# Performance work log

Measured on AMD Instinct MI355X. Metric: run time of the kernel, lower is better.

## Reference

```python
import jax, jax.numpy as jnp
import numpy as np

B, T, K, H = 2, 2048, 1024, 16


def setup_inputs() -> dict:
    key = jax.random.key(0)
    ks = jax.random.split(key, 9)
    sc = 0.02
    return {
        "x": jax.random.normal(ks[0], (B, T, K), dtype=jnp.float32),
        "Wq_w": jax.random.normal(ks[1], (K, K), dtype=jnp.float32) * sc,
        "Wq_b": jax.random.normal(ks[2], (K,), dtype=jnp.float32) * sc,
        "Wk_w": jax.random.normal(ks[3], (K, K), dtype=jnp.float32) * sc,
        "Wk_b": jax.random.normal(ks[4], (K,), dtype=jnp.float32) * sc,
        "Wv_w": jax.random.normal(ks[5], (K, K), dtype=jnp.float32) * sc,
        "Wv_b": jax.random.normal(ks[6], (K,), dtype=jnp.float32) * sc,
        "Wo_w": jax.random.normal(ks[7], (K, K), dtype=jnp.float32) * sc,
        "Wo_b": jax.random.normal(ks[8], (K,), dtype=jnp.float32) * sc,
    }


def reference(x, Wq_w, Wq_b, Wk_w, Wk_b, Wv_w, Wv_b, Wo_w, Wo_b):
    b, t, k = x.shape
    h = H
    s = k // h
    # nn.Linear: y = x @ W^T + b
    q = x @ Wq_w.T + Wq_b
    kk = x @ Wk_w.T + Wk_b
    v = x @ Wv_w.T + Wv_b
    # [b, t, h, s] -> [b, h, t, s]
    q = q.reshape(b, t, h, s).transpose(0, 2, 1, 3)
    kk = kk.reshape(b, t, h, s).transpose(0, 2, 1, 3)
    v = v.reshape(b, t, h, s).transpose(0, 2, 1, 3)
    # scores [b, h, t, t]
    dot = jnp.einsum("bhqd,bhkd->bhqk", q, kk)
    # causal mask: upper triangle (offset=1) set to -inf BEFORE scaling
    causal = jnp.tril(jnp.ones((t, t), dtype=bool))
    dot = jnp.where(causal, dot, -jnp.inf)
    # NOTE: original scales by sqrt(k) (full model dim), not sqrt(head_dim)
    dot = dot / jnp.sqrt(jnp.asarray(k, dot.dtype))
    attn = jax.nn.softmax(dot, axis=-1)
    out = jnp.einsum("bhqk,bhkd->bhqd", attn, v)  # [b, h, t, s]
    out = out.transpose(0, 2, 1, 3).reshape(b, t, k)
    return out @ Wo_w.T + Wo_b
```

## Files before the change

### kernel.cpp

```cpp
#include <hip/hip_runtime.h>

typedef unsigned short u16;
typedef unsigned int u32;
typedef __bf16 bf16x8 __attribute__((ext_vector_type(8)));
typedef float f32x4 __attribute__((ext_vector_type(4)));
typedef unsigned short u16x8 __attribute__((ext_vector_type(8)));
typedef unsigned int u32x4 __attribute__((ext_vector_type(4)));

#define B_ 2
#define T_ 2048
#define K_ 1024
#define H_ 16
#define S_ 64
#define MKC 4194304
#define QSCALE 0.04508422f

__device__ __forceinline__ u16 f2bf(float f) {
  unsigned int u = __builtin_bit_cast(unsigned int, f);
  u += 0x7fffu + ((u >> 16) & 1u);
  return (u16)(u >> 16);
}

__device__ __forceinline__ f32x4 MFMA(bf16x8 a, bf16x8 b, f32x4 c) {
  return __builtin_amdgcn_mfma_f32_16x16x32_bf16(a, b, c, 0, 0, 0);
}

__device__ __forceinline__ void gld16(const void* g, void* l) {
  __builtin_amdgcn_global_load_lds((const __attribute__((address_space(1))) void*)g,
                                   (__attribute__((address_space(3))) void*)l, 16, 0, 0);
}

template <int N>
__device__ __forceinline__ void waitv() {
  asm volatile("s_waitcnt vmcnt(%0)" ::"i"(N) : "memory");
}
__device__ __forceinline__ void memfence_barrier() {
  asm volatile("" ::: "memory");
  __builtin_amdgcn_s_barrier();
}
__device__ __forceinline__ float fmax3(float a, float b, float c) {
  return fmaxf(fmaxf(a, b), c);
}

__global__ __launch_bounds__(256) void cvt_all(const float* __restrict__ x,
                                               const float* __restrict__ W0,
                                               const float* __restrict__ W1,
                                               const float* __restrict__ W2,
                                               const float* __restrict__ W3,
                                               u16* __restrict__ xb,
                                               u16* __restrict__ wb) {
  const int i = blockIdx.x * 256 + threadIdx.x;
  const float* src;
  u16* dst;
  if (i < 524288) {
    src = x + (size_t)i * 8;
    dst = xb + (size_t)i * 8;
  } else {
    const int j = i - 524288;
    const int sel = j >> 17;
    const float* W = sel == 0 ? W0 : sel == 1 ? W1 : sel == 2 ? W2 : W3;
    src = W + (size_t)(j & 131071) * 8;
    dst = wb + (size_t)j * 8;
  }
  const float4* s = (const float4*)src;
  float4 f0 = s[0], f1 = s[1];
  u16x8 p;
  p[0] = f2bf(f0.x); p[1] = f2bf(f0.y); p[2] = f2bf(f0.z); p[3] = f2bf(f0.w);
  p[4] = f2bf(f1.x); p[5] = f2bf(f1.y); p[6] = f2bf(f1.z); p[7] = f2bf(f1.w);
  *(u16x8*)dst = p;
}

template <int OMODE, int BN>
__global__ __launch_bounds__(256) void gemm16(const u16* __restrict__ A,
                                              const u16* __restrict__ Bm,
                                              const float* __restrict__ b0,
                                              const float* __restrict__ b1,
                                              const float* __restrict__ b2,
                                              void* __restrict__ C0,
                                              int M, int N, int K) {
  constexpr int NF = BN / 32;
  constexpr int SOPS = 2 + BN / 64;
  __shared__ u16 As[2][128 * 32];
  __shared__ u16 Bs[2][BN * 32];
  const int bm = blockIdx.x * 128;
  const int bn = blockIdx.y * BN;
  const int tid = threadIdx.x;
  const int w = tid >> 6, lane = tid & 63;
  const int wr = (w >> 1) * 64, wc = (w & 1) * (BN / 2);
  const int lr = lane & 15, g = lane >> 4;
  const int lk = g * 8;
  const int srow = lane >> 2, scol = (lane & 3) * 8;

  f32x4 acc[4][NF] = {};

  auto stg = [&](int buf, int k0) {
#pragma unroll
    for (int i = 0; i < 2; ++i) {
      const int rbase = (i * 4 + w) * 16;
      gld16(A + (size_t)(bm + rbase + srow) * K + k0 + scol, &As[buf][rbase * 32]);
    }
#pragma unroll
    for (int i = 0; i < BN / 64; ++i) {
      const int rbase = (i * 4 + w) * 16;
      gld16(Bm + (size_t)(bn + rbase + srow) * K + k0 + scol, &Bs[buf][rbase * 32]);
    }
  };

  stg(0, 0);
  const int NK = K >> 5;
  for (int kk = 0; kk < NK; ++kk) {
    const int buf = kk & 1;
    const bool pf = (kk + 1 < NK);
    if (pf) {
      stg(buf ^ 1, (kk + 1) * 32);
      waitv<SOPS>();
    } else {
      waitv<0>();
    }
    __builtin_amdgcn_s_barrier();
    bf16x8 af[4], bfr[NF];
#pragma unroll
    for (int m = 0; m < 4; ++m)
      af[m] = *(const bf16x8*)&As[buf][(wr + m * 16 + lr) * 32 + lk];
#pragma unroll
    for (int n = 0; n < NF; ++n)
      bfr[n] = *(const bf16x8*)&Bs[buf][(wc + n * 16 + lr) * 32 + lk];
#pragma unroll
    for (int m = 0; m < 4; ++m)
#pragma unroll
      for (int n = 0; n < NF; ++n)
        acc[m][n] = MFMA(af[m], bfr[n], acc[m][n]);
    memfence_barrier();
  }

  const int sel = (OMODE == 2) ? 0 : (bn >> 10);
  const float* bp = (OMODE == 2) ? b0 : (sel == 0 ? b0 : sel == 1 ? b1 : b2);
#pragma unroll
  for (int n = 0; n < NF; ++n) {
    const int col = bn + wc + n * 16 + lr;
    const float bv = bp[(OMODE == 2) ? col : (col & 1023)];
#pragma unroll
    for (int m = 0; m < 4; ++m) {
#pragma unroll
      for (int r = 0; r < 4; ++r) {
        const int row = bm + wr + m * 16 + g * 4 + r;
        float v = acc[m][n][r] + bv;
        if (OMODE == 2) {
          ((float*)C0)[(size_t)row * N + col] = v;
        } else {
          u16* dst = (u16*)C0;
          const int cc = col & 1023;
          if (sel == 2) {
            const int bb = row >> 11, t = row & 2047, hh = cc >> 6, ss = cc & 63;
            dst[(size_t)2 * MKC + (((size_t)(bb * H_ + hh) * S_ + ss) << 11) + t] = f2bf(v);
          } else {
            if (sel == 0) v *= QSCALE;
            dst[(size_t)sel * MKC + (size_t)row * 1024 + cc] = f2bf(v);
          }
        }
      }
    }
  }
}

__global__ __launch_bounds__(256) void attn_fwd(const u16* __restrict__ Q,
                                                const u16* __restrict__ Kb,
                                                const u16* __restrict__ Vt,
                                                u16* __restrict__ O) {
  __shared__ u16 Ks[2][64 * 64];
  __shared__ u16 Vs[2][64 * 64];
  const int tid = threadIdx.x;
  const int w = tid >> 6, lane = tid & 63;
  const int qh = lane & 15;
  const int g = lane >> 4;
  const int bh = blockIdx.x;
  const int b = bh >> 4, h = bh & 15;
  const int yy = blockIdx.y;

  const int srow = lane >> 3;
  const int sl8 = ((lane & 7) ^ srow) * 8;
  int kvp[2];
#pragma unroll
  for (int i = 0; i < 2; ++i) {
    const int rho = w * 16 + i * 8 + srow;
    const int a = rho >> 4;
    kvp[i] = ((a >> 1) << 5) | (((rho >> 2) & 3) << 3) | ((a & 1) << 2) | (rho & 3);
  }
  const int ksw = qh & 7;
  u16x8 ov;
#pragma unroll
  for (int i = 0; i < 8; ++i) ov[i] = 0x3F80;
  const bf16x8 ones = __builtin_bit_cast(bf16x8, ov);

  for (int seg = 0; seg < 2; ++seg) {
    const int qtile = seg ? (31 - yy) : yy;
    const int qb = qtile * 64;
    const int qw = qb + w * 16;
    const int myq = qw + qh;
    const int nk = qtile + 1;

    const size_t qoff = (size_t)(b * T_ + qw + qh) * K_ + h * S_ + g * 8;
    const bf16x8 bq0 = *(const bf16x8*)(Q + qoff);
    const bf16x8 bq1 = *(const bf16x8*)(Q + qoff + 32);

    const u16* kq0 = Kb + (size_t)(b * T_ + kvp[0]) * K_ + h * S_ + sl8;
    const u16* kq1 = Kb + (size_t)(b * T_ + kvp[1]) * K_ + h * S_ + sl8;
    const u16* vq0 = Vt + (size_t)(bh * S_ + w * 16 + srow) * T_ + sl8;
    const u16* vq1 = Vt + (size_t)(bh * S_ + w * 16 + 8 + srow) * T_ + sl8;

    auto stageK = [&](int buf) {
      gld16(kq0, &Ks[buf][(w * 16) * 64]);
      gld16(kq1, &Ks[buf][(w * 16 + 8) * 64]);
      kq0 += 64 * K_; kq1 += 64 * K_;
    };
    auto stageV = [&](int buf) {
      gld16(vq0, &Vs[buf][(w * 16) * 64]);
      gld16(vq1, &Vs[buf][(w * 16 + 8) * 64]);
      vq0 += 64; vq1 += 64;
    };

    float m = -INFINITY;
    f32x4 o[4] = {};
    f32x4 o_l = {};
    f32x4 sA[4], sB[4];

    auto QKT = [&](int buf, f32x4 (&sO)[4]) {
      __builtin_amdgcn_s_setprio(1);
#pragma unroll
      for (int a = 0; a < 4; ++a) {
        const u16* kr = &Ks[buf][(a * 16 + qh) * 64];
        const bf16x8 kf0 = *(const bf16x8*)(kr + ((g ^ ksw) * 8));
        const bf16x8 kf1 = *(const bf16x8*)(kr + (((4 + g) ^ ksw) * 8));
        f32x4 z = {0.f, 0.f, 0.f, 0.f};
        z = MFMA(kf0, bq0, z);
        sO[a] = MFMA(kf1, bq1, z);
      }
      __builtin_amdgcn_s_setprio(0);
    };

    auto SMPV = [&](f32x4 (&sIn)[4], int buf, int k0) {
      float p[4][4];
      if (k0 + 63 > qw) {
        const int thr = myq - k0 - (g << 3);
#pragma unroll
        for (int a = 0; a < 4; ++a)
#pragma unroll
          for (int r = 0; r < 4; ++r) {
            const int C = ((a >> 1) << 5) + ((a & 1) << 2) + r;
            p[a][r] = (C <= thr) ? sIn[a][r] : -INFINITY;
          }
      } else {
#pragma unroll
        for (int a = 0; a < 4; ++a)
#pragma unroll
          for (int r = 0; r < 4; ++r) p[a][r] = sIn[a][r];
      }
      float x0 = fmax3(p[0][0], p[0][1], p[0][2]);
      float x1 = fmax3(p[0][3], p[1][0], p[1][1]);
      float x2 = fmax3(p[1][2], p[1][3], p[2][0]);
      float x3 = fmax3(p[2][1], p[2][2], p[2][3]);
      float x4 = fmax3(p[3][0], p[3][1], p[3][2]);
      float vmax = fmax3(fmax3(x0, x1, x2), x3, fmaxf(x4, p[3][3]));
      vmax = fmaxf(vmax, __shfl_xor(vmax, 16));
      vmax = fmaxf(vmax, __shfl_xor(vmax, 32));

      if (__any(vmax > m + 11.5f)) {
        const float mnew = fmaxf(m, vmax);
        const float alpha = __builtin_amdgcn_exp2f(m - mnew);
        m = mnew;
        float aR[4];
#pragma unroll
        for (int r = 0; r < 4; ++r) aR[r] = __shfl(alpha, 4 * g + r);
#pragma unroll
        for (int nn = 0; nn < 4; ++nn)
#pragma unroll
          for (int r = 0; r < 4; ++r) o[nn][r] *= aR[r];
#pragma unroll
        for (int r = 0; r < 4; ++r) o_l[r] *= aR[r];
      }

#pragma unroll
      for (int a = 0; a < 4; ++a)
#pragma unroll
        for (int r = 0; r < 4; ++r)
          p[a][r] = __builtin_amdgcn_exp2f(p[a][r] - m);

      __builtin_amdgcn_s_setprio(1);
#pragma unroll
      for (int c = 0; c < 2; ++c) {
        u32 t0, t1, t2, t3;
        asm("v_cvt_pk_bf16_f32 %0, %1, %2" : "=v"(t0) : "v"(p[2 * c][0]), "v"(p[2 * c][1]));
        asm("v_cvt_pk_bf16_f32 %0, %1, %2" : "=v"(t1) : "v"(p[2 * c][2]), "v"(p[2 * c][3]));
        asm("v_cvt_pk_bf16_f32 %0, %1, %2" : "=v"(t2) : "v"(p[2 * c + 1][0]), "v"(p[2 * c + 1][1]));
        asm("v_cvt_pk_bf16_f32 %0, %1, %2" : "=v"(t3) : "v"(p[2 * c + 1][2]), "v"(p[2 * c + 1][3]));
        u32x4 tv; tv[0] = t0; tv[1] = t1; tv[2] = t2; tv[3] = t3;
        const bf16x8 pa = __builtin_bit_cast(bf16x8, tv);
        o_l = MFMA(pa, ones, o_l);
#pragma unroll
        for (int nn = 0; nn < 4; ++nn) {
          const bf16x8 vf =
              *(const bf16x8*)(&Vs[buf][(16 * nn + qh) * 64] + (((c * 4 + g) ^ ksw) * 8));
          o[nn] = MFMA(pa, vf, o[nn]);
        }
      }
      __builtin_amdgcn_s_setprio(0);
    };

    stageK(0); stageV(0);
    waitv<0>();
    __builtin_amdgcn_s_barrier();
    QKT(0, sA);
    if (nk > 1) { stageK(1); stageV(1); }

    int kt = 0;
    for (;;) {
      {
        const bool hn = kt + 1 < nk;
        if (hn) waitv<2>(); else waitv<0>();
        __builtin_amdgcn_s_barrier();
        if (hn) { QKT(1, sB); if (kt + 2 < nk) stageK(0); }
        SMPV(sA, 0, kt * 64);
        memfence_barrier();
        if (kt + 2 < nk) stageV(0);
        if (!hn) break;
        ++kt;
      }
      {
        const bool hn = kt + 1 < nk;
        if (hn) waitv<2>(); else waitv<0>();
        __builtin_amdgcn_s_barrier();
        if (hn) { QKT(0, sA); if (kt + 2 < nk) stageK(1); }
        SMPV(sB, 1, kt * 64);
        memfence_barrier();
        if (kt + 2 < nk) stageV(1);
        if (!hn) break;
        ++kt;
      }
    }

#pragma unroll
    for (int r = 0; r < 4; ++r) {
      const float inv = 1.f / o_l[r];
      const size_t row = (size_t)(b * T_ + qw + 4 * g + r);
#pragma unroll
      for (int nn = 0; nn < 4; ++nn)
        O[row * K_ + h * S_ + nn * 16 + qh] = f2bf(o[nn][r] * inv);
    }
  }
}

extern "C" void kernel_launch(void* const* d_in, const int* in_sizes, int n_in,
                              void* d_out, int out_size, void* d_ws, size_t ws_size,
                              hipStream_t stream) {
  (void)in_sizes; (void)n_in; (void)out_size; (void)ws_size;
  const float* x  = (const float*)d_in[0];
  const float* Wq = (const float*)d_in[1];
  const float* bq = (const float*)d_in[2];
  const float* Wk = (const float*)d_in[3];
  const float* bk = (const float*)d_in[4];
  const float* Wv = (const float*)d_in[5];
  const float* bv = (const float*)d_in[6];
  const float* Wo = (const float*)d_in[7];
  const float* bo = (const float*)d_in[8];
  float* out = (float*)d_out;

  const size_t MK = (size_t)MKC;
  const size_t WK = (size_t)K_ * K_;
  u16* Qb  = (u16*)d_ws;
  u16* Kbf = Qb + MK;
  u16* Vtb = Kbf + MK;
  u16* AO  = Vtb + MK;
  u16* xb  = AO + MK;
  u16* Wqkv = xb + MK;
  u16* Wob  = Wqkv + 3 * WK;

  dim3 blk(256);
  cvt_all<<<dim3(4096), blk, 0, stream>>>(x, Wq, Wk, Wv, Wo, xb, Wqkv);
  gemm16<3, 128><<<dim3(32, 24), blk, 0, stream>>>(xb, Wqkv, bq, bk, bv, Qb,
                                                   B_ * T_, 3 * K_, K_);
  attn_fwd<<<dim3(B_ * H_, 16), blk, 0, stream>>>(Qb, Kbf, Vtb, AO);
  gemm16<2, 64><<<dim3(32, 16), blk, 0, stream>>>(AO, Wob, bo, bo, bo, out,
                                                  B_ * T_, K_, K_);
}
```

Baseline: 105.7 us.

## Split long causal query tiles across two blocks and merge partials

Attention work is rebalanced. Before, each block paired query tile y with tile 31-y. Now the 16 longest query tiles have their KV range split into two halves handled by separate blocks, and the 16 shorter tiles run as single blocks, giving 48 blocks per head instead of 16. Split blocks write normalized bf16 partial outputs plus row max and sum into the reused xb workspace, and a new merge kernel combines them with log-sum-exp weights. The aim is more parallelism and shorter per-block critical paths, at the cost of an extra launch, extra global traffic, and bf16 rounding of the partials.

Result: slower. 110.3 us (+4.4%).

```diff
diff --git a/kernel.cpp b/kernel.cpp
--- a/kernel.cpp
+++ b/kernel.cpp
@@ -14,11 +14,16 @@
 #define S_ 64
 #define MKC 4194304
 #define QSCALE 0.04508422f
+#define PSTRIDE 4352
 
 __device__ __forceinline__ u16 f2bf(float f) {
   unsigned int u = __builtin_bit_cast(unsigned int, f);
   u += 0x7fffu + ((u >> 16) & 1u);
   return (u16)(u >> 16);
+}
+__device__ __forceinline__ float bf2f(u16 u) {
+  u32 x = ((u32)u) << 16;
+  return __builtin_bit_cast(float, x);
 }
 
 __device__ __forceinline__ f32x4 MFMA(bf16x8 a, bf16x8 b, f32x4 c) {
@@ -166,7 +171,8 @@
 __global__ __launch_bounds__(256) void attn_fwd(const u16* __restrict__ Q,
                                                 const u16* __restrict__ Kb,
                                                 const u16* __restrict__ Vt,
-                                                u16* __restrict__ O) {
+                                                u16* __restrict__ O,
+                                                u16* __restrict__ part) {
   __shared__ u16 Ks[2][64 * 64];
   __shared__ u16 Vs[2][64 * 64];
   const int tid = threadIdx.x;
@@ -175,7 +181,25 @@
   const int g = lane >> 4;
   const int bh = blockIdx.x;
   const int b = bh >> 4, h = bh & 15;
-  const int yy = blockIdx.y;
+  const int j = blockIdx.y;
+  int y, k_lo, k_hi;
+  if (j < 32) {
+    y = 31 - (j >> 1);
+    const int h0 = (y + 2) >> 1;
+    k_lo = (j & 1) ? h0 : 0;
+    k_hi = (j & 1) ? (y + 1) : h0;
+  } else {
+    y = 47 - j;
+    k_lo = 0;
+    k_hi = y + 1;
+  }
+  const int qb = y * 64;
+  const int qw = qb + w * 16;
+  const int myq = qw + qh;
+
+  const size_t qoff = (size_t)(b * T_ + qw + qh) * K_ + h * S_ + g * 8;
+  const bf16x8 bq0 = *(const bf16x8*)(Q + qoff);
+  const bf16x8 bq1 = *(const bf16x8*)(Q + qoff + 32);
 
   const int srow = lane >> 3;
   const int sl8 = ((lane & 7) ^ srow) * 8;
@@ -192,152 +216,142 @@
   for (int i = 0; i < 8; ++i) ov[i] = 0x3F80;
   const bf16x8 ones = __builtin_bit_cast(bf16x8, ov);
 
-  for (int seg = 0; seg < 2; ++seg) {
-    const int qtile = seg ? (31 - yy) : yy;
-    const int qb = qtile * 64;
-    const int qw = qb + w * 16;
-    const int myq = qw + qh;
-    const int nk = qtile + 1;
-
-    const size_t qoff = (size_t)(b * T_ + qw + qh) * K_ + h * S_ + g * 8;
-    const bf16x8 bq0 = *(const bf16x8*)(Q + qoff);
-    const bf16x8 bq1 = *(const bf16x8*)(Q + qoff + 32);
-
-    const u16* kq0 = Kb + (size_t)(b * T_ + kvp[0]) * K_ + h * S_ + sl8;
-    const u16* kq1 = Kb + (size_t)(b * T_ + kvp[1]) * K_ + h * S_ + sl8;
-    const u16* vq0 = Vt + (size_t)(bh * S_ + w * 16 + srow) * T_ + sl8;
-    const u16* vq1 = Vt + (size_t)(bh * S_ + w * 16 + 8 + srow) * T_ + sl8;
-
-    auto stageK = [&](int buf) {
-      gld16(kq0, &Ks[buf][(w * 16) * 64]);
-      gld16(kq1, &Ks[buf][(w * 16 + 8) * 64]);
-      kq0 += 64 * K_; kq1 += 64 * K_;
-    };
-    auto stageV = [&](int buf) {
-      gld16(vq0, &Vs[buf][(w * 16) * 64]);
-      gld16(vq1, &Vs[buf][(w * 16 + 8) * 64]);
-      vq0 += 64; vq1 += 64;
-    };
-
-    float m = -INFINITY;
-    f32x4 o[4] = {};
-    f32x4 o_l = {};
-    f32x4 sA[4], sB[4];
-
-    auto QKT = [&](int buf, f32x4 (&sO)[4]) {
-      __builtin_amdgcn_s_setprio(1);
-#pragma unroll
-      for (int a = 0; a < 4; ++a) {
-        const u16* kr = &Ks[buf][(a * 16 + qh) * 64];
-        const bf16x8 kf0 = *(const bf16x8*)(kr + ((g ^ ksw) * 8));
-        const bf16x8 kf1 = *(const bf16x8*)(kr + (((4 + g) ^ ksw) * 8));
-        f32x4 z = {0.f, 0.f, 0.f, 0.f};
-        z = MFMA(kf0, bq0, z);
-        sO[a] = MFMA(kf1, bq1, z);
+  const u16* kq0 = Kb + (size_t)(b * T_ + k_lo * 64 + kvp[0]) * K_ + h * S_ + sl8;
+  const u16* kq1 = Kb + (size_t)(b * T_ + k_lo * 64 + kvp[1]) * K_ + h * S_ + sl8;
+  const u16* vq0 = Vt + (size_t)(bh * S_ + w * 16 + srow) * T_ + k_lo * 64 + sl8;
+  const u16* vq1 = Vt + (size_t)(bh * S_ + w * 16 + 8 + srow) * T_ + k_lo * 64 + sl8;
+
+  auto stageK = [&](int buf) {
+    gld16(kq0, &Ks[buf][(w * 16) * 64]);
+    gld16(kq1, &Ks[buf][(w * 16 + 8) * 64]);
+    kq0 += 64 * K_; kq1 += 64 * K_;
+  };
+  auto stageV = [&](int buf) {
+    gld16(vq0, &Vs[buf][(w * 16) * 64]);
+    gld16(vq1, &Vs[buf][(w * 16 + 8) * 64]);
+    vq0 += 64; vq1 += 64;
+  };
+
+  float m = -INFINITY;
+  f32x4 o[4] = {};
+  f32x4 o_l = {};
+  f32x4 sA[4], sB[4];
+
+  auto QKT = [&](int buf, f32x4 (&sO)[4]) {
+    __builtin_amdgcn_s_setprio(1);
+#pragma unroll
+    for (int a = 0; a < 4; ++a) {
+      const u16* kr = &Ks[buf][(a * 16 + qh) * 64];
+      const bf16x8 kf0 = *(const bf16x8*)(kr + ((g ^ ksw) * 8));
+      const bf16x8 kf1 = *(const bf16x8*)(kr + (((4 + g) ^ ksw) * 8));
+      f32x4 z = {0.f, 0.f, 0.f, 0.f};
+      z = MFMA(kf0, bq0, z);
+      sO[a] = MFMA(kf1, bq1, z);
+    }
+    __builtin_amdgcn_s_setprio(0);
+  };
+
+  auto SMPV = [&](f32x4 (&sIn)[4], int buf, int k0) {
+    float p[4][4];
+    if (k0 + 63 > qw) {
+      const int thr = myq - k0 - (g << 3);
+#pragma unroll
+      for (int a = 0; a < 4; ++a)
+#pragma unroll
+        for (int r = 0; r < 4; ++r) {
+          const int C = ((a >> 1) << 5) + ((a & 1) << 2) + r;
+          p[a][r] = (C <= thr) ? sIn[a][r] : -INFINITY;
+        }
+    } else {
+#pragma unroll
+      for (int a = 0; a < 4; ++a)
+#pragma unroll
+        for (int r = 0; r < 4; ++r) p[a][r] = sIn[a][r];
+    }
+    float x0 = fmax3(p[0][0], p[0][1], p[0][2]);
+    float x1 = fmax3(p[0][3], p[1][0], p[1][1]);
+    float x2 = fmax3(p[1][2], p[1][3], p[2][0]);
+    float x3 = fmax3(p[2][1], p[2][2], p[2][3]);
+    float x4 = fmax3(p[3][0], p[3][1], p[3][2]);
+    float vmax = fmax3(fmax3(x0, x1, x2), x3, fmaxf(x4, p[3][3]));
+    vmax = fmaxf(vmax, __shfl_xor(vmax, 16));
+    vmax = fmaxf(vmax, __shfl_xor(vmax, 32));
+
+    if (__any(vmax > m + 11.5f)) {
+      const float mnew = fmaxf(m, vmax);
+      const float alpha = __builtin_amdgcn_exp2f(m - mnew);
+      m = mnew;
+      float aR[4];
+#pragma unroll
+      for (int r = 0; r < 4; ++r) aR[r] = __shfl(alpha, 4 * g + r);
+#pragma unroll
+      for (int nn = 0; nn < 4; ++nn)
+#pragma unroll
+        for (int r = 0; r < 4; ++r) o[nn][r] *= aR[r];
+#pragma unroll
+      for (int r = 0; r < 4; ++r) o_l[r] *= aR[r];
+    }
+
+#pragma unroll
+    for (int a = 0; a < 4; ++a)
+#pragma unroll
+      for (int r = 0; r < 4; ++r)
+        p[a][r] = __builtin_amdgcn_exp2f(p[a][r] - m);
+
+    __builtin_amdgcn_s_setprio(1);
+#pragma unroll
+    for (int c = 0; c < 2; ++c) {
+      u32 t0, t1, t2, t3;
+      asm("v_cvt_pk_bf16_f32 %0, %1, %2" : "=v"(t0) : "v"(p[2 * c][0]), "v"(p[2 * c][1]));
+      asm("v_cvt_pk_bf16_f32 %0, %1, %2" : "=v"(t1) : "v"(p[2 * c][2]), "v"(p[2 * c][3]));
+      asm("v_cvt_pk_bf16_f32 %0, %1, %2" : "=v"(t2) : "v"(p[2 * c + 1][0]), "v"(p[2 * c + 1][1]));
+      asm("v_cvt_pk_bf16_f32 %0, %1, %2" : "=v"(t3) : "v"(p[2 * c + 1][2]), "v"(p[2 * c + 1][3]));
+      u32x4 tv; tv[0] = t0; tv[1] = t1; tv[2] = t2; tv[3] = t3;
+      const bf16x8 pa = __builtin_bit_cast(bf16x8, tv);
+      o_l = MFMA(pa, ones, o_l);
+#pragma unroll
+      for (int nn = 0; nn < 4; ++nn) {
+        const bf16x8 vf =
+            *(const bf16x8*)(&Vs[buf][(16 * nn + qh) * 64] + (((c * 4 + g) ^ ksw) * 8));
+        o[nn] = MFMA(pa, vf, o[nn]);
       }
-      __builtin_amdgcn_s_setprio(0);
-    };
-
-    auto SMPV = [&](f32x4 (&sIn)[4], int buf, int k0) {
-      float p[4][4];
-      if (k0 + 63 > qw) {
-        const int thr = myq - k0 - (g << 3);
-#pragma unroll
-        for (int a = 0; a < 4; ++a)
-#pragma unroll
-          for (int r = 0; r < 4; ++r) {
-            const int C = ((a >> 1) << 5) + ((a & 1) << 2) + r;
-            p[a][r] = (C <= thr) ? sIn[a][r] : -INFINITY;
-          }
-      } else {
-#pragma unroll
-        for (int a = 0; a < 4; ++a)
-#pragma unroll
-          for (int r = 0; r < 4; ++r) p[a][r] = sIn[a][r];
-      }
-      float x0 = fmax3(p[0][0], p[0][1], p[0][2]);
-      float x1 = fmax3(p[0][3], p[1][0], p[1][1]);
-      float x2 = fmax3(p[1][2], p[1][3], p[2][0]);
-      float x3 = fmax3(p[2][1], p[2][2], p[2][3]);
-      float x4 = fmax3(p[3][0], p[3][1], p[3][2]);
-      float vmax = fmax3(fmax3(x0, x1, x2), x3, fmaxf(x4, p[3][3]));
-      vmax = fmaxf(vmax, __shfl_xor(vmax, 16));
-      vmax = fmaxf(vmax, __shfl_xor(vmax, 32));
-
-      if (__any(vmax > m + 11.5f)) {
-        const float mnew = fmaxf(m, vmax);
-        const float alpha = __builtin_amdgcn_exp2f(m - mnew);
-        m = mnew;
-        float aR[4];
-#pragma unroll
-        for (int r = 0; r < 4; ++r) aR[r] = __shfl(alpha, 4 * g + r);
-#pragma unroll
-        for (int nn = 0; nn < 4; ++nn)
-#pragma unroll
-          for (int r = 0; r < 4; ++r) o[nn][r] *= aR[r];
-#pragma unroll
-        for (int r = 0; r < 4; ++r) o_l[r] *= aR[r];
-      }
-
-#pragma unroll
-      for (int a = 0; a < 4; ++a)
-#pragma unroll
-        for (int r = 0; r < 4; ++r)
-          p[a][r] = __builtin_amdgcn_exp2f(p[a][r] - m);
-
-      __builtin_amdgcn_s_setprio(1);
-#pragma unroll
-      for (int c = 0; c < 2; ++c) {
-        u32 t0, t1, t2, t3;
-        asm("v_cvt_pk_bf16_f32 %0, %1, %2" : "=v"(t0) : "v"(p[2 * c][0]), "v"(p[2 * c][1]));
-        asm("v_cvt_pk_bf16_f32 %0, %1, %2" : "=v"(t1) : "v"(p[2 * c][2]), "v"(p[2 * c][3]));
-        asm("v_cvt_pk_bf16_f32 %0, %1, %2" : "=v"(t2) : "v"(p[2 * c + 1][0]), "v"(p[2 * c + 1][1]));
-        asm("v_cvt_pk_bf16_f32 %0, %1, %2" : "=v"(t3) : "v"(p[2 * c + 1][2]), "v"(p[2 * c + 1][3]));
-        u32x4 tv; tv[0] = t0; tv[1] = t1; tv[2] = t2; tv[3] = t3;
-        const bf16x8 pa = __builtin_bit_cast(bf16x8, tv);
-        o_l = MFMA(pa, ones, o_l);
-#pragma unroll
-        for (int nn = 0; nn < 4; ++nn) {
-          const bf16x8 vf =
-              *(const bf16x8*)(&Vs[buf][(16 * nn + qh) * 64] + (((c * 4 + g) ^ ksw) * 8));
-          o[nn] = MFMA(pa, vf, o[nn]);
-        }
-      }
-      __builtin_amdgcn_s_setprio(0);
-    };
-
-    stageK(0); stageV(0);
-    waitv<0>();
-    __builtin_amdgcn_s_barrier();
-    QKT(0, sA);
-    if (nk > 1) { stageK(1); stageV(1); }
-
-    int kt = 0;
-    for (;;) {
-      {
-        const bool hn = kt + 1 < nk;
-        if (hn) waitv<2>(); else waitv<0>();
-        __builtin_amdgcn_s_barrier();
-        if (hn) { QKT(1, sB); if (kt + 2 < nk) stageK(0); }
-        SMPV(sA, 0, kt * 64);
-        memfence_barrier();
-        if (kt + 2 < nk) stageV(0);
-        if (!hn) break;
-        ++kt;
-      }
-      {
-        const bool hn = kt + 1 < nk;
-        if (hn) waitv<2>(); else waitv<0>();
-        __builtin_amdgcn_s_barrier();
-        if (hn) { QKT(0, sA); if (kt + 2 < nk) stageK(1); }
-        SMPV(sB, 1, kt * 64);
-        memfence_barrier();
-        if (kt + 2 < nk) stageV(1);
-        if (!hn) break;
-        ++kt;
-      }
-    }
-
+    }
+    __builtin_amdgcn_s_setprio(0);
+  };
+
+  stageK(0); stageV(0);
+  waitv<0>();
+  __builtin_amdgcn_s_barrier();
+  QKT(0, sA);
+  if (k_lo + 1 < k_hi) { stageK(1); stageV(1); }
+
+  int kt = k_lo;
+  for (;;) {
+    {
+      const bool hn = kt + 1 < k_hi;
+      if (hn) waitv<2>(); else waitv<0>();
+      __builtin_amdgcn_s_barrier();
+      if (hn) { QKT(1, sB); if (kt + 2 < k_hi) stageK(0); }
+      SMPV(sA, 0, kt * 64);
+      memfence_barrier();
+      if (kt + 2 < k_hi) stageV(0);
+      if (!hn) break;
+      ++kt;
+    }
+    {
+      const bool hn = kt + 1 < k_hi;
+      if (hn) waitv<2>(); else waitv<0>();
+      __builtin_amdgcn_s_barrier();
+      if (hn) { QKT(0, sA); if (kt + 2 < k_hi) stageK(1); }
+      SMPV(sB, 1, kt * 64);
+      memfence_barrier();
+      if (kt + 2 < k_hi) stageV(1);
+      if (!hn) break;
+      ++kt;
+    }
+  }
+
+  if (j >= 32) {
 #pragma unroll
     for (int r = 0; r < 4; ++r) {
       const float inv = 1.f / o_l[r];
@@ -346,7 +360,61 @@
       for (int nn = 0; nn < 4; ++nn)
         O[row * K_ + h * S_ + nn * 16 + qh] = f2bf(o[nn][r] * inv);
     }
-  }
+  } else {
+    const int slot = j * 32 + bh;
+    u16* po = part + (size_t)slot * PSTRIDE;
+    float* ps = (float*)(po + 4096);
+#pragma unroll
+    for (int r = 0; r < 4; ++r) {
+      const float inv = 1.f / o_l[r];
+      const int ri = w * 16 + 4 * g + r;
+#pragma unroll
+      for (int nn = 0; nn < 4; ++nn)
+        po[ri * 64 + nn * 16 + qh] = f2bf(o[nn][r] * inv);
+    }
+    if (g == 0) ps[w * 16 + qh] = m;
+    if (qh < 4) {
+      float lv = o_l[0];
+      if (qh == 1) lv = o_l[1];
+      else if (qh == 2) lv = o_l[2];
+      else if (qh == 3) lv = o_l[3];
+      ps[64 + w * 16 + 4 * g + qh] = lv;
+    }
+  }
+}
+
+__global__ __launch_bounds__(256) void merge_attn(const u16* __restrict__ part,
+                                                  u16* __restrict__ AO) {
+  const int bh = blockIdx.x;
+  const int y = 16 + blockIdx.y;
+  const int b = bh >> 4, h = bh & 15;
+  const int t = threadIdx.x;
+  const int row = t >> 2, cg = t & 3;
+  const u16* p0 = part + (size_t)((2 * (31 - y)) * 32 + bh) * PSTRIDE;
+  const u16* p1 = p0 + (size_t)32 * PSTRIDE;
+  const float* s0 = (const float*)(p0 + 4096);
+  const float* s1 = (const float*)(p1 + 4096);
+  const float m0 = s0[row], l0 = s0[64 + row];
+  const float m1 = s1[row], l1 = s1[64 + row];
+  const float M = fmaxf(m0, m1);
+  const float a0 = __builtin_amdgcn_exp2f(m0 - M) * l0;
+  const float a1 = __builtin_amdgcn_exp2f(m1 - M) * l1;
+  const float dn = 1.f / (a0 + a1);
+  const float w0 = a0 * dn, w1 = a1 * dn;
+  const int co = row * 64 + cg * 16;
+  u16x8 o0a = *(const u16x8*)(p0 + co);
+  u16x8 o0b = *(const u16x8*)(p0 + co + 8);
+  u16x8 o1a = *(const u16x8*)(p1 + co);
+  u16x8 o1b = *(const u16x8*)(p1 + co + 8);
+  u16x8 ra, rb;
+#pragma unroll
+  for (int i = 0; i < 8; ++i) {
+    ra[i] = f2bf(w0 * bf2f(o0a[i]) + w1 * bf2f(o1a[i]));
+    rb[i] = f2bf(w0 * bf2f(o0b[i]) + w1 * bf2f(o1b[i]));
+  }
+  u16* dst = AO + (size_t)(b * T_ + y * 64 + row) * K_ + h * S_ + cg * 16;
+  *(u16x8*)dst = ra;
+  *(u16x8*)(dst + 8) = rb;
 }
 
 extern "C" void kernel_launch(void* const* d_in, const int* in_sizes, int n_in,
@@ -378,7 +446,8 @@
   cvt_all<<<dim3(4096), blk, 0, stream>>>(x, Wq, Wk, Wv, Wo, xb, Wqkv);
   gemm16<3, 128><<<dim3(32, 24), blk, 0, stream>>>(xb, Wqkv, bq, bk, bv, Qb,
                                                    B_ * T_, 3 * K_, K_);
-  attn_fwd<<<dim3(B_ * H_, 16), blk, 0, stream>>>(Qb, Kbf, Vtb, AO);
+  attn_fwd<<<dim3(B_ * H_, 48), blk, 0, stream>>>(Qb, Kbf, Vtb, AO, xb);
+  merge_attn<<<dim3(B_ * H_, 16), blk, 0, stream>>>(xb, AO);
   gemm16<2, 64><<<dim3(32, 16), blk, 0, stream>>>(AO, Wob, bo, bo, bo, out,
                                                   B_ * T_, K_, K_);
 }
```
